# Optimization experiments

Measured on AMD Instinct MI355X. Metric: run time of the kernel, lower is better.

The kernel has to match this reference:

```python
import jax, jax.numpy as jnp
import numpy as np

V = 50257   # vocab_size
E = 768     # embed_dim
NH = 12     # num_heads
HD = E // NH
L = 4       # num_layers
T = 1024    # seq_len == max_seq_len
B = 2       # batch
FF = 4 * E  # ffn hidden
EPS = 1e-5


def _layernorm(x, scale, bias):
    m = jnp.mean(x, axis=-1, keepdims=True)
    v = jnp.var(x, axis=-1, keepdims=True)
    return (x - m) * jax.lax.rsqrt(v + EPS) * scale + bias


def setup_inputs() -> dict:
    key = jax.random.key(0)
    ks = jax.random.split(key, 12)
    s = 0.02
    d = {}
    d["input_ids"] = jax.random.randint(ks[0], (B, T), 0, V)
    d["tok_emb"] = jax.random.normal(ks[1], (V, E), jnp.float32) * s
    d["pos_emb"] = jax.random.normal(ks[2], (T, E), jnp.float32) * s
    d["ln1_scale"] = jnp.ones((L, E), jnp.float32)
    d["ln1_bias"] = jnp.zeros((L, E), jnp.float32)
    d["qkv_w"] = jax.random.normal(ks[3], (L, 3 * E, E), jnp.float32) * s
    d["out_w"] = jax.random.normal(ks[4], (L, E, E), jnp.float32) * s
    d["ln2_scale"] = jnp.ones((L, E), jnp.float32)
    d["ln2_bias"] = jnp.zeros((L, E), jnp.float32)
    d["fc1_w"] = jax.random.normal(ks[5], (L, FF, E), jnp.float32) * s
    d["fc1_b"] = jnp.zeros((L, FF), jnp.float32)
    d["fc2_w"] = jax.random.normal(ks[6], (L, E, FF), jnp.float32) * s
    d["fc2_b"] = jnp.zeros((L, E), jnp.float32)
    d["lnf_scale"] = jnp.ones((E,), jnp.float32)
    d["lnf_bias"] = jnp.zeros((E,), jnp.float32)
    return d


def reference(input_ids, tok_emb, pos_emb, ln1_scale, ln1_bias, qkv_w, out_w,
              ln2_scale, ln2_bias, fc1_w, fc1_b, fc2_w, fc2_b, lnf_scale, lnf_bias):
    Bc, Tc = input_ids.shape
    scale = HD ** -0.5
    x = tok_emb[input_ids] + pos_emb[:Tc]            # (B,T,E); dropout p=0 (eval)
    causal = jnp.triu(jnp.ones((Tc, Tc), bool), 1)   # True above diagonal -> masked
    neg_inf = jnp.finfo(x.dtype).min

    for l in range(L):
        # --- causal self-attention (pre-norm) ---
        h = _layernorm(x, ln1_scale[l], ln1_bias[l])
        qkv = h @ qkv_w[l].T                         # (B,T,3E)
        q, k, v = jnp.split(qkv, 3, axis=-1)
        q = q.reshape(Bc, Tc, NH, HD)
        k = k.reshape(Bc, Tc, NH, HD)
        v = v.reshape(Bc, Tc, NH, HD)
        attn = jnp.einsum('bqhd,bkhd->bhqk', q, k) * scale
        attn = jnp.where(causal, neg_inf, attn)
        attn = jax.nn.softmax(attn, axis=-1)
        o = jnp.einsum('bhqk,bkhd->bqhd', attn, v).reshape(Bc, Tc, E)
        x = x + o @ out_w[l].T
        # --- GELU FFN (pre-norm) ---
        h = _layernorm(x, ln2_scale[l], ln2_bias[l])
        h = jax.nn.gelu(h @ fc1_w[l].T + fc1_b[l], approximate=False)
        x = x + h @ fc2_w[l].T + fc2_b[l]

    x = _layernorm(x, lnf_scale, lnf_bias)
    logits = x @ tok_emb.T                           # tied LM head
    return logits
```

## Files before the change

kernel.cpp:

```cpp
#include <hip/hip_runtime.h>
#include <hip/hip_bf16.h>
#include <math.h>

#define E_DIM 768
#define T_SEQ 1024
#define B_SZ  2
#define NHEAD 12
#define HDIM  64
#define NLAY  4
#define FF_DIM 3072
#define VOCAB 50257
#define M_ROWS 2048

typedef short bf16x8 __attribute__((ext_vector_type(8)));
typedef float floatx4 __attribute__((ext_vector_type(4)));

__device__ __forceinline__ unsigned short f2bf(float f) {
    union { __hip_bfloat16 h; unsigned short u; } cv;
    cv.h = __float2bfloat16(f);
    return cv.u;
}

__device__ __forceinline__ void gload_lds16(const unsigned short* g, void* l) {
    __builtin_amdgcn_global_load_lds(
        (const __attribute__((address_space(1))) void*)g,
        (__attribute__((address_space(3))) void*)l, 16, 0, 0);
}

__global__ __launch_bounds__(256) void f32_to_bf16(
    const float* __restrict__ src, unsigned short* __restrict__ dst, int n8)
{
    int i = blockIdx.x * 256 + threadIdx.x;
    int stride = gridDim.x * 256;
    for (; i < n8; i += stride) {
        const float4* s = (const float4*)(src + (size_t)i * 8);
        float4 a = s[0], b = s[1];
        union { unsigned short u[8]; uint4 v; } cv;
        cv.u[0] = f2bf(a.x); cv.u[1] = f2bf(a.y); cv.u[2] = f2bf(a.z); cv.u[3] = f2bf(a.w);
        cv.u[4] = f2bf(b.x); cv.u[5] = f2bf(b.y); cv.u[6] = f2bf(b.z); cv.u[7] = f2bf(b.w);
        *(uint4*)(dst + (size_t)i * 8) = cv.v;
    }
}

__global__ __launch_bounds__(256) void embed_kernel(
    const int* __restrict__ ids, const float* __restrict__ tok,
    const float* __restrict__ pos, float* __restrict__ x)
{
    int row = blockIdx.x;
    int t = row & (T_SEQ - 1);
    int id = ids[row];
    const float* te = tok + (size_t)id * E_DIM;
    const float* pe = pos + (size_t)t * E_DIM;
    float* xr = x + (size_t)row * E_DIM;
    for (int e = threadIdx.x; e < E_DIM; e += 256) xr[e] = te[e] + pe[e];
}

__global__ __launch_bounds__(256) void ln_kernel(
    const float* __restrict__ x, const float* __restrict__ scale,
    const float* __restrict__ bias, unsigned short* __restrict__ out)
{
    int row = blockIdx.x;
    const float* xr = x + (size_t)row * E_DIM;
    int tid = threadIdx.x;
    float v0 = xr[tid], v1 = xr[tid + 256], v2 = xr[tid + 512];
    float s  = v0 + v1 + v2;
    float sq = v0 * v0 + v1 * v1 + v2 * v2;
    for (int o = 32; o; o >>= 1) {
        s  += __shfl_down(s,  o, 64);
        sq += __shfl_down(sq, o, 64);
    }
    __shared__ float red[8];
    int wid = tid >> 6;
    if ((tid & 63) == 0) { red[wid] = s; red[wid + 4] = sq; }
    __syncthreads();
    float ts = red[0] + red[1] + red[2] + red[3];
    float tq = red[4] + red[5] + red[6] + red[7];
    float mean = ts * (1.0f / E_DIM);
    float var  = tq * (1.0f / E_DIM) - mean * mean;
    float rstd = rsqrtf(var + 1e-5f);
    unsigned short* orow = out + (size_t)row * E_DIM;
    orow[tid]       = f2bf((v0 - mean) * rstd * scale[tid]       + bias[tid]);
    orow[tid + 256] = f2bf((v1 - mean) * rstd * scale[tid + 256] + bias[tid + 256]);
    orow[tid + 512] = f2bf((v2 - mean) * rstd * scale[tid + 512] + bias[tid + 512]);
}

__global__ __launch_bounds__(256) void gemm_bb(
    const unsigned short* __restrict__ A, const unsigned short* __restrict__ W,
    float* __restrict__ outf, unsigned short* __restrict__ outb,
    const float* __restrict__ bias, const float* __restrict__ resid,
    int K, int N, int do_gelu)
{
    __shared__ __align__(16) unsigned short As[128 * 32];
    __shared__ __align__(16) unsigned short Bs[128 * 32];
    const int tid = threadIdx.x;
    const int bm = blockIdx.x, bn = blockIdx.y;
    const int lane = tid & 63, wid = tid >> 6;
    const int quad = lane >> 4, l16 = lane & 15;
    const int wm = wid >> 1, wn = wid & 1;

    floatx4 acc[4][4];
    #pragma unroll
    for (int mt = 0; mt < 4; ++mt)
        #pragma unroll
        for (int nt = 0; nt < 4; ++nt) acc[mt][nt] = (floatx4)0.0f;

    const int srow = lane >> 2;
    const int scol = (lane & 3) * 8;
    const unsigned short* aptr0 = A + (size_t)(bm * 128 + wid * 16 + srow) * K + scol;
    const unsigned short* aptr1 = aptr0 + (size_t)64 * K;
    int wr0 = bn * 128 + wid * 16 + srow;
    int wr1 = wr0 + 64;
    if (wr0 >= N) wr0 = N - 1;
    if (wr1 >= N) wr1 = N - 1;
    const unsigned short* wptr0 = W + (size_t)wr0 * K + scol;
    const unsigned short* wptr1 = W + (size_t)wr1 * K + scol;
    char* lA = (char*)As + (wid << 10);
    char* lB = (char*)Bs + (wid << 10);

    for (int k0 = 0; k0 < K; k0 += 32) {
        __syncthreads();
        gload_lds16(aptr0 + k0, lA);
        gload_lds16(aptr1 + k0, lA + 4096);
        gload_lds16(wptr0 + k0, lB);
        gload_lds16(wptr1 + k0, lB + 4096);
        __syncthreads();

        bf16x8 af[4], bfr[4];
        #pragma unroll
        for (int mt = 0; mt < 4; ++mt)
            af[mt] = *(const bf16x8*)&As[(wm * 64 + mt * 16 + l16) * 32 + quad * 8];
        #pragma unroll
        for (int nt = 0; nt < 4; ++nt)
            bfr[nt] = *(const bf16x8*)&Bs[(wn * 64 + nt * 16 + l16) * 32 + quad * 8];
        #pragma unroll
        for (int mt = 0; mt < 4; ++mt)
            #pragma unroll
            for (int nt = 0; nt < 4; ++nt)
                acc[mt][nt] = __builtin_amdgcn_mfma_f32_16x16x32_bf16(
                    af[mt], bfr[nt], acc[mt][nt], 0, 0, 0);
    }

    #pragma unroll
    for (int mt = 0; mt < 4; ++mt) {
        #pragma unroll
        for (int nt = 0; nt < 4; ++nt) {
            int col = bn * 128 + wn * 64 + nt * 16 + l16;
            if (col >= N) continue;
            float bv = bias ? bias[col] : 0.0f;
            #pragma unroll
            for (int r = 0; r < 4; ++r) {
                int row = bm * 128 + wm * 64 + mt * 16 + quad * 4 + r;
                float v = acc[mt][nt][r] + bv;
                if (do_gelu) v = 0.5f * v * (1.0f + erff(v * 0.70710678118654752f));
                size_t idx = (size_t)row * N + col;
                if (resid) v += resid[idx];
                if (outf) outf[idx] = v;
                else      outb[idx] = f2bf(v);
            }
        }
    }
}

__global__ __launch_bounds__(256) void gemm_bt(
    const unsigned short* __restrict__ A, const float* __restrict__ W,
    float* __restrict__ outf, unsigned short* __restrict__ outb,
    const float* __restrict__ bias, const float* __restrict__ resid,
    int K, int N, int do_gelu)
{
    __shared__ __align__(16) unsigned short As[128 * 40];
    __shared__ __align__(16) unsigned short Bs[128 * 40];
    const int tid = threadIdx.x;
    const int bm = blockIdx.y, bn = blockIdx.x;
    const int lane = tid & 63, wid = tid >> 6;
    const int quad = lane >> 4, l16 = lane & 15;
    const int wm = wid >> 1, wn = wid & 1;

    floatx4 acc[4][4];
    #pragma unroll
    for (int mt = 0; mt < 4; ++mt)
        #pragma unroll
        for (int nt = 0; nt < 4; ++nt) acc[mt][nt] = (floatx4)0.0f;

    for (int k0 = 0; k0 < K; k0 += 32) {
        __syncthreads();
        #pragma unroll
        for (int i = 0; i < 2; ++i) {
            int c = tid + i * 256;
            int r = c >> 2, c8 = (c & 3) * 8;
            *(uint4*)&As[r * 40 + c8] =
                *(const uint4*)&A[(size_t)(bm * 128 + r) * K + k0 + c8];
        }
        #pragma unroll
        for (int i = 0; i < 2; ++i) {
            int c = tid + i * 256;
            int r = c >> 2, c8 = (c & 3) * 8;
            int gn = bn * 128 + r;
            float f[8];
            if (gn < N) {
                const float* src = &W[(size_t)gn * K + k0 + c8];
                float4 a0 = *(const float4*)src;
                float4 a1 = *(const float4*)(src + 4);
                f[0] = a0.x; f[1] = a0.y; f[2] = a0.z; f[3] = a0.w;
                f[4] = a1.x; f[5] = a1.y; f[6] = a1.z; f[7] = a1.w;
            } else {
                #pragma unroll
                for (int j = 0; j < 8; ++j) f[j] = 0.0f;
            }
            union { unsigned short u[8]; uint4 v; } cv;
            #pragma unroll
            for (int j = 0; j < 8; ++j) cv.u[j] = f2bf(f[j]);
            *(uint4*)&Bs[r * 40 + c8] = cv.v;
        }
        __syncthreads();

        bf16x8 af[4], bfr[4];
        #pragma unroll
        for (int mt = 0; mt < 4; ++mt)
            af[mt] = *(const bf16x8*)&As[(wm * 64 + mt * 16 + l16) * 40 + quad * 8];
        #pragma unroll
        for (int nt = 0; nt < 4; ++nt)
            bfr[nt] = *(const bf16x8*)&Bs[(wn * 64 + nt * 16 + l16) * 40 + quad * 8];
        #pragma unroll
        for (int mt = 0; mt < 4; ++mt)
            #pragma unroll
            for (int nt = 0; nt < 4; ++nt)
                acc[mt][nt] = __builtin_amdgcn_mfma_f32_16x16x32_bf16(
                    af[mt], bfr[nt], acc[mt][nt], 0, 0, 0);
    }

    #pragma unroll
    for (int mt = 0; mt < 4; ++mt) {
        #pragma unroll
        for (int nt = 0; nt < 4; ++nt) {
            int col = bn * 128 + wn * 64 + nt * 16 + l16;
            if (col >= N) continue;
            float bv = bias ? bias[col] : 0.0f;
            #pragma unroll
            for (int r = 0; r < 4; ++r) {
                int row = bm * 128 + wm * 64 + mt * 16 + quad * 4 + r;
                float v = acc[mt][nt][r] + bv;
                if (do_gelu) v = 0.5f * v * (1.0f + erff(v * 0.70710678118654752f));
                size_t idx = (size_t)row * N + col;
                if (resid) v += resid[idx];
                if (outf) outf[idx] = v;
                else      outb[idx] = f2bf(v);
            }
        }
    }
}

__global__ __launch_bounds__(256) void attn_kernel(
    const unsigned short* __restrict__ qkv, unsigned short* __restrict__ attno)
{
    __shared__ __align__(16) unsigned short Qs[64 * 88];
    __shared__ __align__(16) unsigned short Ks[64 * 88];
    __shared__ __align__(16) unsigned short Vt[64 * 88];
    __shared__ __align__(16) unsigned short Ps[4][16 * 88];

    const int tid = threadIdx.x;
    const int qtile = blockIdx.x;
    const int h = blockIdx.y;
    const int b = blockIdx.z;
    const int lane = tid & 63, wid = tid >> 6;
    const int quad = lane >> 4, l16 = lane & 15;

    #pragma unroll
    for (int i = 0; i < 2; ++i) {
        int c = tid + i * 256;
        int r = c >> 3, c8 = (c & 7) * 8;
        int row = b * T_SEQ + qtile * 64 + r;
        *(uint4*)&Qs[r * 88 + c8] =
            *(const uint4*)&qkv[(size_t)row * (3 * E_DIM) + h * HDIM + c8];
    }

    float m_i[4], l_i[4];
    floatx4 acco[4];
    #pragma unroll
    for (int r = 0; r < 4; ++r) { m_i[r] = -INFINITY; l_i[r] = 0.0f; }
    #pragma unroll
    for (int dt = 0; dt < 4; ++dt) acco[dt] = (floatx4)0.0f;

    for (int kt = 0; kt <= qtile; ++kt) {
        __syncthreads();
        #pragma unroll
        for (int i = 0; i < 2; ++i) {
            int c = tid + i * 256;
            int r = c >> 3, c8 = (c & 7) * 8;
            int row = b * T_SEQ + kt * 64 + r;
            *(uint4*)&Ks[r * 88 + c8] =
                *(const uint4*)&qkv[(size_t)row * (3 * E_DIM) + E_DIM + h * HDIM + c8];
        }
        {
            int t = tid >> 2, d0 = (tid & 3) * 16;
            int row = b * T_SEQ + kt * 64 + t;
            const unsigned short* src =
                &qkv[(size_t)row * (3 * E_DIM) + 2 * E_DIM + h * HDIM + d0];
            unsigned short tmp[16];
            *(uint4*)&tmp[0] = *(const uint4*)src;
            *(uint4*)&tmp[8] = *(const uint4*)(src + 8);
            #pragma unroll
            for (int j = 0; j < 16; ++j) Vt[(d0 + j) * 88 + t] = tmp[j];
        }
        __syncthreads();

        floatx4 accs[4];
        #pragma unroll
        for (int ct = 0; ct < 4; ++ct) accs[ct] = (floatx4)0.0f;
        #pragma unroll
        for (int ct = 0; ct < 4; ++ct)
            #pragma unroll
            for (int kk = 0; kk < 64; kk += 32) {
                bf16x8 a  = *(const bf16x8*)&Qs[(wid * 16 + l16) * 88 + kk + quad * 8];
                bf16x8 bb = *(const bf16x8*)&Ks[(ct * 16 + l16) * 88 + kk + quad * 8];
                accs[ct] = __builtin_amdgcn_mfma_f32_16x16x32_bf16(a, bb, accs[ct], 0, 0, 0);
            }

        float p[4][4];
        #pragma unroll
        for (int ct = 0; ct < 4; ++ct)
            #pragma unroll
            for (int r = 0; r < 4; ++r) {
                float s = accs[ct][r] * 0.125f;
                int kg = kt * 64 + ct * 16 + l16;
                int qg = qtile * 64 + wid * 16 + quad * 4 + r;
                p[ct][r] = (kg > qg) ? -INFINITY : s;
            }
        float alpha[4];
        #pragma unroll
        for (int r = 0; r < 4; ++r) {
            float rm = fmaxf(fmaxf(p[0][r], p[1][r]), fmaxf(p[2][r], p[3][r]));
            for (int m = 1; m < 16; m <<= 1) rm = fmaxf(rm, __shfl_xor(rm, m, 64));
            float mn = fmaxf(m_i[r], rm);
            alpha[r] = __expf(m_i[r] - mn);
            float rs = 0.0f;
            #pragma unroll
            for (int ct = 0; ct < 4; ++ct) {
                p[ct][r] = __expf(p[ct][r] - mn);
                rs += p[ct][r];
            }
            for (int m = 1; m < 16; m <<= 1) rs += __shfl_xor(rs, m, 64);
            l_i[r] = l_i[r] * alpha[r] + rs;
            m_i[r] = mn;
        }
        #pragma unroll
        for (int ct = 0; ct < 4; ++ct)
            #pragma unroll
            for (int r = 0; r < 4; ++r)
                Ps[wid][(quad * 4 + r) * 88 + ct * 16 + l16] = f2bf(p[ct][r]);
        #pragma unroll
        for (int dt = 0; dt < 4; ++dt)
            #pragma unroll
            for (int r = 0; r < 4; ++r) acco[dt][r] *= alpha[r];
        __syncthreads();
        #pragma unroll
        for (int dt = 0; dt < 4; ++dt)
            #pragma unroll
            for (int kk = 0; kk < 64; kk += 32) {
                bf16x8 a  = *(const bf16x8*)&Ps[wid][l16 * 88 + kk + quad * 8];
                bf16x8 bb = *(const bf16x8*)&Vt[(dt * 16 + l16) * 88 + kk + quad * 8];
                acco[dt] = __builtin_amdgcn_mfma_f32_16x16x32_bf16(a, bb, acco[dt], 0, 0, 0);
            }
    }

    #pragma unroll
    for (int dt = 0; dt < 4; ++dt)
        #pragma unroll
        for (int r = 0; r < 4; ++r) {
            int trow = qtile * 64 + wid * 16 + quad * 4 + r;
            float v = acco[dt][r] / l_i[r];
            attno[(size_t)(b * T_SEQ + trow) * E_DIM + h * HDIM + dt * 16 + l16] = f2bf(v);
        }
}

extern "C" void kernel_launch(void* const* d_in, const int* in_sizes, int n_in,
                              void* d_out, int out_size, void* d_ws, size_t ws_size,
                              hipStream_t stream)
{
    const int*   ids  = (const int*)d_in[0];
    const float* tok  = (const float*)d_in[1];
    const float* pos  = (const float*)d_in[2];
    const float* ln1s = (const float*)d_in[3];
    const float* ln1b = (const float*)d_in[4];
    const float* qkvw = (const float*)d_in[5];
    const float* outw = (const float*)d_in[6];
    const float* ln2s = (const float*)d_in[7];
    const float* ln2b = (const float*)d_in[8];
    const float* fc1w = (const float*)d_in[9];
    const float* fc1b = (const float*)d_in[10];
    const float* fc2w = (const float*)d_in[11];
    const float* fc2b = (const float*)d_in[12];
    const float* lnfs = (const float*)d_in[13];
    const float* lnfb = (const float*)d_in[14];

    char* ws = (char*)d_ws;
    float*          x     = (float*)ws;
    unsigned short* hbuf  = (unsigned short*)(ws + 6291456);
    unsigned short* qkvb  = (unsigned short*)(ws + 9437184);
    unsigned short* attno = (unsigned short*)(ws + 18874368);
    unsigned short* ffnb  = (unsigned short*)(ws + 22020096);
    unsigned short* tokb  = (unsigned short*)(ws + 34603008);
    unsigned short* qkvwb = (unsigned short*)(ws + 111797760);
    unsigned short* outwb = (unsigned short*)(ws + 125953536);
    unsigned short* fc1wb = (unsigned short*)(ws + 130672128);
    unsigned short* fc2wb = (unsigned short*)(ws + 149546496);
    const bool big = ws_size >= 168420864ull;

    if (big) {
        f32_to_bf16<<<2048, 256, 0, stream>>>(tok,  tokb,  VOCAB * E_DIM / 8);
        f32_to_bf16<<<2048, 256, 0, stream>>>(qkvw, qkvwb, NLAY * 3 * E_DIM * E_DIM / 8);
        f32_to_bf16<<<2048, 256, 0, stream>>>(outw, outwb, NLAY * E_DIM * E_DIM / 8);
        f32_to_bf16<<<2048, 256, 0, stream>>>(fc1w, fc1wb, NLAY * FF_DIM * E_DIM / 8);
        f32_to_bf16<<<2048, 256, 0, stream>>>(fc2w, fc2wb, NLAY * E_DIM * FF_DIM / 8);
    }

    embed_kernel<<<M_ROWS, 256, 0, stream>>>(ids, tok, pos, x);

    for (int l = 0; l < NLAY; ++l) {
        ln_kernel<<<M_ROWS, 256, 0, stream>>>(x, ln1s + l * E_DIM, ln1b + l * E_DIM, hbuf);
        if (big)
            gemm_bb<<<dim3(16, 18), 256, 0, stream>>>(
                hbuf, qkvwb + (size_t)l * 3 * E_DIM * E_DIM, nullptr, qkvb,
                nullptr, nullptr, E_DIM, 3 * E_DIM, 0);
        else
            gemm_bt<<<dim3(18, 16), 256, 0, stream>>>(
                hbuf, qkvw + (size_t)l * 3 * E_DIM * E_DIM, nullptr, qkvb,
                nullptr, nullptr, E_DIM, 3 * E_DIM, 0);
        attn_kernel<<<dim3(16, NHEAD, B_SZ), 256, 0, stream>>>(qkvb, attno);
        if (big)
            gemm_bb<<<dim3(16, 6), 256, 0, stream>>>(
                attno, outwb + (size_t)l * E_DIM * E_DIM, x, nullptr,
                nullptr, x, E_DIM, E_DIM, 0);
        else
            gemm_bt<<<dim3(6, 16), 256, 0, stream>>>(
                attno, outw + (size_t)l * E_DIM * E_DIM, x, nullptr,
                nullptr, x, E_DIM, E_DIM, 0);
        ln_kernel<<<M_ROWS, 256, 0, stream>>>(x, ln2s + l * E_DIM, ln2b + l * E_DIM, hbuf);
        if (big) {
            gemm_bb<<<dim3(16, 24), 256, 0, stream>>>(
                hbuf, fc1wb + (size_t)l * FF_DIM * E_DIM, nullptr, ffnb,
                fc1b + l * FF_DIM, nullptr, E_DIM, FF_DIM, 1);
            gemm_bb<<<dim3(16, 6), 256, 0, stream>>>(
                ffnb, fc2wb + (size_t)l * E_DIM * FF_DIM, x, nullptr,
                fc2b + l * E_DIM, x, FF_DIM, E_DIM, 0);
        } else {
            gemm_bt<<<dim3(24, 16), 256, 0, stream>>>(
                hbuf, fc1w + (size_t)l * FF_DIM * E_DIM, nullptr, ffnb,
                fc1b + l * FF_DIM, nullptr, E_DIM, FF_DIM, 1);
            gemm_bt<<<dim3(6, 16), 256, 0, stream>>>(
                ffnb, fc2w + (size_t)l * E_DIM * FF_DIM, x, nullptr,
                fc2b + l * E_DIM, x, FF_DIM, E_DIM, 0);
        }
    }

    ln_kernel<<<M_ROWS, 256, 0, stream>>>(x, lnfs, lnfb, hbuf);
    if (big)
        gemm_bb<<<dim3(16, (VOCAB + 127) / 128), 256, 0, stream>>>(
            hbuf, tokb, (float*)d_out, nullptr, nullptr, nullptr, E_DIM, VOCAB, 0);
    else
        gemm_bt<<<dim3((VOCAB + 127) / 128, 16), 256, 0, stream>>>(
            hbuf, tok, (float*)d_out, nullptr, nullptr, nullptr, E_DIM, VOCAB, 0);
}
```

Measured before the change: 1.833 ms.

## Double-buffer LDS tiles in bf16 GEMM to overlap loads with MFMA

Splits the GEMM's shared-memory A/B tiles into two buffers. The next K-slice is loaded directly to LDS while MFMAs run on the current buffer, and one barrier per step replaces two. The goal is to hide global-load latency behind compute. It doubles LDS use to 32KB per block, which may reduce occupancy, and the loop assumes the number of K steps is even.

After: 1.791 ms. 2.3% less time.

```diff
diff --git a/kernel.cpp b/kernel.cpp
--- a/kernel.cpp
+++ b/kernel.cpp
@@ -90,8 +90,8 @@
     const float* __restrict__ bias, const float* __restrict__ resid,
     int K, int N, int do_gelu)
 {
-    __shared__ __align__(16) unsigned short As[128 * 32];
-    __shared__ __align__(16) unsigned short Bs[128 * 32];
+    __shared__ __align__(16) unsigned short As[2][128 * 32];
+    __shared__ __align__(16) unsigned short Bs[2][128 * 32];
     const int tid = threadIdx.x;
     const int bm = blockIdx.x, bn = blockIdx.y;
     const int lane = tid & 63, wid = tid >> 6;
@@ -114,31 +114,51 @@
     if (wr1 >= N) wr1 = N - 1;
     const unsigned short* wptr0 = W + (size_t)wr0 * K + scol;
     const unsigned short* wptr1 = W + (size_t)wr1 * K + scol;
-    char* lA = (char*)As + (wid << 10);
-    char* lB = (char*)Bs + (wid << 10);
-
-    for (int k0 = 0; k0 < K; k0 += 32) {
-        __syncthreads();
-        gload_lds16(aptr0 + k0, lA);
-        gload_lds16(aptr1 + k0, lA + 4096);
-        gload_lds16(wptr0 + k0, lB);
-        gload_lds16(wptr1 + k0, lB + 4096);
-        __syncthreads();
-
-        bf16x8 af[4], bfr[4];
-        #pragma unroll
-        for (int mt = 0; mt < 4; ++mt)
-            af[mt] = *(const bf16x8*)&As[(wm * 64 + mt * 16 + l16) * 32 + quad * 8];
-        #pragma unroll
-        for (int nt = 0; nt < 4; ++nt)
-            bfr[nt] = *(const bf16x8*)&Bs[(wn * 64 + nt * 16 + l16) * 32 + quad * 8];
-        #pragma unroll
-        for (int mt = 0; mt < 4; ++mt)
-            #pragma unroll
-            for (int nt = 0; nt < 4; ++nt)
-                acc[mt][nt] = __builtin_amdgcn_mfma_f32_16x16x32_bf16(
-                    af[mt], bfr[nt], acc[mt][nt], 0, 0, 0);
-    }
+    char* lA0 = (char*)As[0] + (wid << 10);
+    char* lA1 = (char*)As[1] + (wid << 10);
+    char* lB0 = (char*)Bs[0] + (wid << 10);
+    char* lB1 = (char*)Bs[1] + (wid << 10);
+
+    #define STAGE_BB(k0, dA, dB)                     \
+        do {                                         \
+            gload_lds16(aptr0 + (k0), (dA));         \
+            gload_lds16(aptr1 + (k0), (dA) + 4096);  \
+            gload_lds16(wptr0 + (k0), (dB));         \
+            gload_lds16(wptr1 + (k0), (dB) + 4096);  \
+        } while (0)
+
+    #define COMPUTE_BB(buf)                                                            \
+        do {                                                                           \
+            const unsigned short* Ac = As[buf];                                        \
+            const unsigned short* Bc = Bs[buf];                                        \
+            bf16x8 af[4], bfr[4];                                                      \
+            _Pragma("unroll")                                                          \
+            for (int mt = 0; mt < 4; ++mt)                                             \
+                af[mt] = *(const bf16x8*)&Ac[(wm * 64 + mt * 16 + l16) * 32 + quad * 8];\
+            _Pragma("unroll")                                                          \
+            for (int nt = 0; nt < 4; ++nt)                                             \
+                bfr[nt] = *(const bf16x8*)&Bc[(wn * 64 + nt * 16 + l16) * 32 + quad * 8];\
+            _Pragma("unroll")                                                          \
+            for (int mt = 0; mt < 4; ++mt)                                             \
+                _Pragma("unroll")                                                      \
+                for (int nt = 0; nt < 4; ++nt)                                         \
+                    acc[mt][nt] = __builtin_amdgcn_mfma_f32_16x16x32_bf16(             \
+                        af[mt], bfr[nt], acc[mt][nt], 0, 0, 0);                        \
+        } while (0)
+
+    const int nsteps = K >> 5;
+    STAGE_BB(0, lA0, lB0);
+    __syncthreads();
+    for (int t = 0; t < nsteps; t += 2) {
+        STAGE_BB((t + 1) << 5, lA1, lB1);
+        COMPUTE_BB(0);
+        __syncthreads();
+        if (t + 2 < nsteps) STAGE_BB((t + 2) << 5, lA0, lB0);
+        COMPUTE_BB(1);
+        __syncthreads();
+    }
+    #undef STAGE_BB
+    #undef COMPUTE_BB
 
     #pragma unroll
     for (int mt = 0; mt < 4; ++mt) {
```
